# Kernel tuning notes

Measured on AMD Instinct MI355X. Metric: run time of the kernel, lower is better.

The kernel has to match this reference:

```python
import jax, jax.numpy as jnp
import numpy as np

B = 32; C = 3; IMG = 224; P = 16; G = IMG // P  # 14x14 patches
N = G * G + 1  # 197 tokens incl cls
D = 768; L = 12; H = 12; HD = D // H; FF = 4 * D
NR = (2 * G - 1) * (2 * G - 1) + 3  # 732
SCALE = HD ** -0.5


def _rel_index():
    ch = np.arange(G); cw = np.arange(G)
    coords = np.stack(np.meshgrid(ch, cw, indexing='ij')).reshape(2, -1)
    rel = (coords[:, :, None] - coords[:, None, :]).transpose(1, 2, 0).copy()
    rel[:, :, 0] += G - 1
    rel[:, :, 1] += G - 1
    rel[:, :, 0] *= 2 * G - 1
    idx = np.zeros((N, N), dtype=np.int32)
    idx[1:, 1:] = rel.sum(-1)
    idx[0, :] = NR - 3
    idx[:, 0] = NR - 2
    idx[0, 0] = NR - 1
    return jnp.asarray(idx)


def setup_inputs() -> dict:
    key = jax.random.key(0)
    ks = jax.random.split(key, 10)
    def nrm(k, shape, s=0.02):
        return jax.random.normal(k, shape, jnp.float32) * s
    return {
        'x': jax.random.normal(ks[0], (B, C, IMG, IMG), jnp.float32),
        'patch_w': nrm(ks[1], (D, C, P, P)),
        'patch_b': jnp.zeros((D,), jnp.float32),
        'cls_token': nrm(ks[2], (1, 1, D)),
        'ln1_g': jnp.ones((L, D), jnp.float32), 'ln1_b': jnp.zeros((L, D), jnp.float32),
        'qkv_w': nrm(ks[3], (L, 3 * D, D)),
        'q_bias': jnp.zeros((L, D), jnp.float32), 'v_bias': jnp.zeros((L, D), jnp.float32),
        'rel_table': nrm(ks[4], (L, NR, H)),
        'proj_w': nrm(ks[5], (L, D, D)), 'proj_b': jnp.zeros((L, D), jnp.float32),
        'gamma1': 0.1 * jnp.ones((L, D), jnp.float32),
        'ln2_g': jnp.ones((L, D), jnp.float32), 'ln2_b': jnp.zeros((L, D), jnp.float32),
        'fc1_w': nrm(ks[6], (L, FF, D)), 'fc1_b': jnp.zeros((L, FF), jnp.float32),
        'fc2_w': nrm(ks[7], (L, D, FF)), 'fc2_b': jnp.zeros((L, D), jnp.float32),
        'gamma2': 0.1 * jnp.ones((L, D), jnp.float32),
        'fcn_g': jnp.ones((D,), jnp.float32), 'fcn_b': jnp.zeros((D,), jnp.float32),
        'rel_index': _rel_index(),
    }


def _ln(x, g, b):
    m = x.mean(-1, keepdims=True)
    v = ((x - m) ** 2).mean(-1, keepdims=True)
    return (x - m) * jax.lax.rsqrt(v + 1e-5) * g + b


def reference(x, patch_w, patch_b, cls_token, ln1_g, ln1_b, qkv_w, q_bias, v_bias,
              rel_table, proj_w, proj_b, gamma1, ln2_g, ln2_b, fc1_w, fc1_b,
              fc2_w, fc2_b, gamma2, fcn_g, fcn_b, rel_index):
    b = x.shape[0]
    # patch embed: stride-P conv == unfold + matmul
    xp = x.reshape(b, C, G, P, G, P).transpose(0, 2, 4, 1, 3, 5).reshape(b, G * G, C * P * P)
    tok = xp @ patch_w.reshape(D, C * P * P).T + patch_b  # [B, 196, D]
    tok = jnp.concatenate([jnp.broadcast_to(cls_token, (b, 1, D)), tok], axis=1)  # [B, N, D]

    def block(t, p):
        g1, b1, qw, qb, vb, rt, pw, pb, gm1, g2, b2, f1w, f1b, f2w, f2b, gm2 = p
        h = _ln(t, g1, b1)
        qkv_bias = jnp.concatenate([qb, jnp.zeros_like(qb), vb])
        qkv = (h @ qw.T + qkv_bias).reshape(b, N, 3, H, HD).transpose(2, 0, 3, 1, 4)
        q, k, v = qkv[0] * SCALE, qkv[1], qkv[2]  # [B,H,N,HD]
        rpb = jnp.transpose(rt[rel_index], (2, 0, 1))  # [H,N,N]
        attn = jax.nn.softmax(jnp.einsum('bhid,bhjd->bhij', q, k) + rpb[None], axis=-1)
        o = jnp.einsum('bhij,bhjd->bhid', attn, v).transpose(0, 2, 1, 3).reshape(b, N, D)
        t = t + gm1 * (o @ pw.T + pb)
        h2 = _ln(t, g2, b2)
        m = jax.nn.gelu(h2 @ f1w.T + f1b, approximate=False) @ f2w.T + f2b
        return t + gm2 * m, None

    params = (ln1_g, ln1_b, qkv_w, q_bias, v_bias, rel_table, proj_w, proj_b,
              gamma1, ln2_g, ln2_b, fc1_w, fc1_b, fc2_w, fc2_b, gamma2)
    tok, _ = jax.lax.scan(block, tok, params)
    # BEiT-style mean pooling over patch tokens + fc_norm
    return _ln(tok[:, 1:].mean(axis=1), fcn_g, fcn_b)  # [B, D]
```

## Files before the change

kernel.cpp:

```cpp
#include <hip/hip_runtime.h>


#define BATCH 32
#define NTOK 197
#define NLAYER 12
#define NRR 732
#define MROWS (BATCH * NTOK)
#define MPAD 6400

#define NKV 224
#define QT_N 13
#define VSTR 232
#define PSTR 232
#define RPB_PER_LH (QT_N * 14 * 4 * 16 * 4)
#define RPB_PER_L (RPB_PER_LH * 12)
#define WL_ELEMS 8257536

typedef __attribute__((ext_vector_type(8))) short bf16x8_t;
typedef __attribute__((ext_vector_type(4))) float f32x4_t;

__device__ __forceinline__ unsigned short f2bf_rn(float f) {
  unsigned u = __float_as_uint(f);
  unsigned r = (u + 0x7FFFu + ((u >> 16) & 1u)) >> 16;
  return (unsigned short)r;
}
__device__ __forceinline__ float bf2f(unsigned short u) {
  return __uint_as_float(((unsigned)u) << 16);
}

__device__ __forceinline__ void gld16(const unsigned short* g, unsigned short* l) {
  __builtin_amdgcn_global_load_lds(
      (const __attribute__((address_space(1))) unsigned int*)g,
      (__attribute__((address_space(3))) unsigned int*)l, 16, 0, 0);
}

__global__ void cvt4(const float4* __restrict__ s, ushort4* __restrict__ d, int n4) {
  int i = blockIdx.x * 256 + threadIdx.x;
  if (i >= n4) return;
  float4 v = s[i];
  ushort4 r;
  r.x = f2bf_rn(v.x); r.y = f2bf_rn(v.y); r.z = f2bf_rn(v.z); r.w = f2bf_rn(v.w);
  d[i] = r;
}

__global__ void cvt_layer(const float4* __restrict__ qw, const float4* __restrict__ pw,
                          const float4* __restrict__ f1, const float4* __restrict__ f2,
                          ushort4* __restrict__ dst) {
  const int n_q = 2304 * 768 / 4;
  const int n_p = 768 * 768 / 4;
  const int n_1 = 3072 * 768 / 4;
  int i = blockIdx.x * 256 + threadIdx.x;
  float4 v;
  if (i < n_q) v = qw[i];
  else if (i < n_q + n_p) v = pw[i - n_q];
  else if (i < n_q + n_p + n_1) v = f1[i - n_q - n_p];
  else if (i < n_q + n_p + 2 * n_1) v = f2[i - n_q - n_p - n_1];
  else return;
  ushort4 r;
  r.x = f2bf_rn(v.x); r.y = f2bf_rn(v.y); r.z = f2bf_rn(v.z); r.w = f2bf_rn(v.w);
  dst[i] = r;
}

__global__ void build_rpb(const float* __restrict__ rt, const int* __restrict__ ridx,
                          unsigned short* __restrict__ dst) {
  int idx = blockIdx.x * 256 + threadIdx.x;
  if (idx >= RPB_PER_L * NLAYER) return;
  int r = idx & 3;
  int fr = (idx >> 2) & 15;
  int fq = (idx >> 6) & 3;
  int t2 = idx >> 8;
  int jt = t2 % 14; t2 /= 14;
  int qt = t2 % QT_N; t2 /= QT_N;
  int h = t2 % 12;
  int l = t2 / 12;
  int row = qt * 16 + fq * 4 + r;
  int col = jt * 16 + fr;
  float v = -30000.f;
  if (row < 197 && col < 197)
    v = rt[((size_t)l * NRR + ridx[row * 197 + col]) * 12 + h];
  dst[idx] = f2bf_rn(v);
}

__global__ void build_xp(const float* __restrict__ x, unsigned short* __restrict__ xp) {
  int idx = blockIdx.x * 256 + threadIdx.x;
  if (idx >= 6272 * 768) return;
  int r = idx / 768, c = idx - r * 768;
  int b = r / 196, p = r - b * 196;
  int gy = p / 14, gx = p - gy * 14;
  int ch = c >> 8, rem = c & 255, py = rem >> 4, px = rem & 15;
  float v = x[(((size_t)b * 3 + ch) * 224 + gy * 16 + py) * 224 + gx * 16 + px];
  xp[(size_t)(b * 197 + 1 + p) * 768 + c] = f2bf_rn(v);
}

__global__ void fill_cls(const float* __restrict__ cls, float* __restrict__ tok) {
  int idx = blockIdx.x * 256 + threadIdx.x;
  int b = idx / 768, d = idx - b * 768;
  tok[(size_t)(b * 197) * 768 + d] = cls[d];
}

__global__ __launch_bounds__(256) void ln_rows(const float* __restrict__ x,
                                               unsigned short* __restrict__ y,
                                               const float* __restrict__ g,
                                               const float* __restrict__ b) {
  int row = blockIdx.x;
  const float* xr = x + (size_t)row * 768;
  int t = threadIdx.x;
  float v0 = xr[t], v1 = xr[t + 256], v2 = xr[t + 512];
  float s = v0 + v1 + v2;
  float q = v0 * v0 + v1 * v1 + v2 * v2;
  for (int off = 32; off; off >>= 1) { s += __shfl_xor(s, off); q += __shfl_xor(q, off); }
  __shared__ float rs[4], rq[4];
  int wave = t >> 6;
  if ((t & 63) == 0) { rs[wave] = s; rq[wave] = q; }
  __syncthreads();
  s = rs[0] + rs[1] + rs[2] + rs[3];
  q = rq[0] + rq[1] + rq[2] + rq[3];
  float mean = s * (1.f / 768.f);
  float var = q * (1.f / 768.f) - mean * mean;
  float rstd = rsqrtf(var + 1e-5f);
  unsigned short* yr = y + (size_t)row * 768;
  yr[t]       = f2bf_rn((v0 - mean) * rstd * g[t]       + b[t]);
  yr[t + 256] = f2bf_rn((v1 - mean) * rstd * g[t + 256] + b[t + 256]);
  yr[t + 512] = f2bf_rn((v2 - mean) * rstd * g[t + 512] + b[t + 512]);
}

template <int MODE, int BM>
__global__ __launch_bounds__(256, 2) void gemm_t(
    const unsigned short* __restrict__ A, const unsigned short* __restrict__ Bw,
    float* __restrict__ Cf, unsigned short* __restrict__ Cb,
    const float* __restrict__ bias, const float* __restrict__ bias2,
    const float* __restrict__ gamma, int K, int N) {
  constexpr int MI = BM / 32;
  __shared__ __align__(16) unsigned short As[2][BM * 32];
  __shared__ __align__(16) unsigned short Bs[2][128 * 32];
  const int tid = threadIdx.x;
  const int wave = tid >> 6, lane = tid & 63;
  const int m0 = blockIdx.y * BM, n0 = blockIdx.x * 128;
  const int wm = (wave & 1) * (MI * 16), wn = (wave >> 1) * 64;
  f32x4_t acc[MI][4] = {};
  const int srow = lane >> 2;
  const int scol = ((lane & 3) ^ ((lane >> 3) & 3)) * 8;
  const unsigned short* Abase = A + (size_t)(m0 + srow) * K + scol;
  const unsigned short* Bbase = Bw + (size_t)(n0 + srow) * K + scol;
  const int fr = lane & 15, fq = lane >> 4;
  const int rchunk = (fq ^ ((fr >> 1) & 3)) * 8;
  for (int k0 = 0; k0 < K; k0 += 64) {
    __syncthreads();
#pragma unroll
    for (int s = 0; s < 2; ++s) {
#pragma unroll
      for (int u0 = 0; u0 < BM / 64; ++u0) {
        int u = wave + u0 * 4;
        gld16(Abase + (size_t)(u * 16) * K + k0 + s * 32, &As[s][u * 512]);
      }
#pragma unroll
      for (int u0 = 0; u0 < 2; ++u0) {
        int u = wave + u0 * 4;
        gld16(Bbase + (size_t)(u * 16) * K + k0 + s * 32, &Bs[s][u * 512]);
      }
    }
    __syncthreads();
#pragma unroll
    for (int s = 0; s < 2; ++s) {
      bf16x8_t af[MI], bfr[4];
#pragma unroll
      for (int i = 0; i < MI; ++i)
        af[i] = *(const bf16x8_t*)(&As[s][(wm + i * 16 + fr) * 32 + rchunk]);
#pragma unroll
      for (int j = 0; j < 4; ++j)
        bfr[j] = *(const bf16x8_t*)(&Bs[s][(wn + j * 16 + fr) * 32 + rchunk]);
#pragma unroll
      for (int i = 0; i < MI; ++i)
#pragma unroll
        for (int j = 0; j < 4; ++j)
          acc[i][j] = __builtin_amdgcn_mfma_f32_16x16x32_bf16(af[i], bfr[j], acc[i][j], 0, 0, 0);
    }
  }
  const int er = (lane >> 4) * 4;
  const int ec = lane & 15;
#pragma unroll
  for (int i = 0; i < MI; ++i) {
#pragma unroll
    for (int j = 0; j < 4; ++j) {
#pragma unroll
      for (int r = 0; r < 4; ++r) {
        int row = m0 + wm + i * 16 + er + r;
        int col = n0 + wn + j * 16 + ec;
        float v = acc[i][j][r];
        size_t idx = (size_t)row * N + col;
        if constexpr (MODE == 0) {
          Cf[idx] = v + bias[col];
        } else if constexpr (MODE == 1) {
          float bv = (col < 768) ? bias[col] : (col >= 1536 ? bias2[col - 1536] : 0.f);
          v += bv;
          if (col < 768) v *= 0.125f;
          Cb[idx] = f2bf_rn(v);
        } else if constexpr (MODE == 2) {
          Cf[idx] = Cf[idx] + gamma[col] * (v + bias[col]);
        } else {
          float tt = v + bias[col];
          float gv = 0.5f * tt * (1.f + erff(tt * 0.70710678118654752f));
          Cb[idx] = f2bf_rn(gv);
        }
      }
    }
  }
}

__global__ __launch_bounds__(256) void attn_mfma(
    const unsigned short* __restrict__ qkv,
    const unsigned short* __restrict__ rpb,
    unsigned short* __restrict__ o) {
  const int bh = blockIdx.x;
  const int b = bh / 12, h = bh - b * 12;
  __shared__ __align__(16) unsigned short Vt[64 * VSTR];
  __shared__ __align__(16) unsigned short Pls[4][16 * PSTR];
  const int t = threadIdx.x;
  const int wave = t >> 6, lane = t & 63;
  const int fr = lane & 15, fq = lane >> 4;
  const size_t qbase = (size_t)(b * 197) * 2304 + h * 64;
  const unsigned short* rph = rpb + (size_t)h * RPB_PER_LH;

  for (int idx = t; idx < NKV * 16; idx += 256) {
    int j = idx >> 4, d0 = (idx & 15) * 4;
    ushort4 v = *(const ushort4*)(qkv + qbase + 1536 + (size_t)j * 2304 + d0);
    Vt[(d0 + 0) * VSTR + j] = v.x;
    Vt[(d0 + 1) * VSTR + j] = v.y;
    Vt[(d0 + 2) * VSTR + j] = v.z;
    Vt[(d0 + 3) * VSTR + j] = v.w;
  }
  __syncthreads();

  unsigned short* P = &Pls[wave][0];
  for (int qt = wave; qt < QT_N; qt += 4) {
    const unsigned short* qrow = qkv + qbase + (size_t)(qt * 16 + fr) * 2304 + fq * 8;
    bf16x8_t qa0 = *(const bf16x8_t*)(qrow);
    bf16x8_t qa1 = *(const bf16x8_t*)(qrow + 32);
    f32x4_t S[14];
#pragma unroll
    for (int jt = 0; jt < 14; ++jt) {
      const unsigned short* krow = qkv + qbase + 768 + (size_t)(jt * 16 + fr) * 2304 + fq * 8;
      bf16x8_t kb0 = *(const bf16x8_t*)(krow);
      bf16x8_t kb1 = *(const bf16x8_t*)(krow + 32);
      f32x4_t s = {};
      s = __builtin_amdgcn_mfma_f32_16x16x32_bf16(qa0, kb0, s, 0, 0, 0);
      s = __builtin_amdgcn_mfma_f32_16x16x32_bf16(qa1, kb1, s, 0, 0, 0);
      ushort4 rb = *(const ushort4*)(rph + ((size_t)(qt * 14 + jt) * 4 + fq) * 64 + fr * 4);
      s[0] += bf2f(rb.x); s[1] += bf2f(rb.y); s[2] += bf2f(rb.z); s[3] += bf2f(rb.w);
      S[jt] = s;
    }
    float mx[4], sum[4];
#pragma unroll
    for (int r = 0; r < 4; ++r) mx[r] = S[0][r];
#pragma unroll
    for (int jt = 1; jt < 14; ++jt)
#pragma unroll
      for (int r = 0; r < 4; ++r) mx[r] = fmaxf(mx[r], S[jt][r]);
#pragma unroll
    for (int r = 0; r < 4; ++r) {
      for (int off = 1; off < 16; off <<= 1) mx[r] = fmaxf(mx[r], __shfl_xor(mx[r], off));
      sum[r] = 0.f;
    }
#pragma unroll
    for (int jt = 0; jt < 14; ++jt) {
#pragma unroll
      for (int r = 0; r < 4; ++r) {
        float p = __expf(S[jt][r] - mx[r]);
        sum[r] += p;
        P[(fq * 4 + r) * PSTR + jt * 16 + fr] = f2bf_rn(p);
      }
    }
    float rinv[4];
#pragma unroll
    for (int r = 0; r < 4; ++r) {
      for (int off = 1; off < 16; off <<= 1) sum[r] += __shfl_xor(sum[r], off);
      rinv[r] = 1.f / sum[r];
    }
    bf16x8_t pa[7];
#pragma unroll
    for (int ks = 0; ks < 7; ++ks)
      pa[ks] = *(const bf16x8_t*)(P + fr * PSTR + ks * 32 + fq * 8);
#pragma unroll
    for (int nt = 0; nt < 4; ++nt) {
      f32x4_t O = {};
#pragma unroll
      for (int ks = 0; ks < 7; ++ks) {
        bf16x8_t vb = *(const bf16x8_t*)(Vt + (nt * 16 + fr) * VSTR + ks * 32 + fq * 8);
        O = __builtin_amdgcn_mfma_f32_16x16x32_bf16(pa[ks], vb, O, 0, 0, 0);
      }
#pragma unroll
      for (int r = 0; r < 4; ++r) {
        int row = qt * 16 + fq * 4 + r;
        if (row < 197)
          o[(size_t)(b * 197 + row) * 768 + h * 64 + nt * 16 + fr] = f2bf_rn(O[r] * rinv[r]);
      }
    }
  }
}

__global__ __launch_bounds__(256) void pool_ln(const float* __restrict__ tok,
                                               const float* __restrict__ g,
                                               const float* __restrict__ bb,
                                               float* __restrict__ out) {
  int b = blockIdx.x;
  __shared__ float pool[768];
  int t = threadIdx.x;
  for (int c = t; c < 768; c += 256) {
    float s = 0.f;
    const float* p = tok + (size_t)(b * 197 + 1) * 768 + c;
    for (int i = 0; i < 196; ++i) s += p[(size_t)i * 768];
    pool[c] = s * (1.f / 196.f);
  }
  __syncthreads();
  float s = 0.f, q = 0.f;
  for (int c = t; c < 768; c += 256) { float v = pool[c]; s += v; q += v * v; }
  for (int off = 32; off; off >>= 1) { s += __shfl_xor(s, off); q += __shfl_xor(q, off); }
  __shared__ float rs[4], rq[4];
  if ((t & 63) == 0) { rs[t >> 6] = s; rq[t >> 6] = q; }
  __syncthreads();
  s = rs[0] + rs[1] + rs[2] + rs[3];
  q = rq[0] + rq[1] + rq[2] + rq[3];
  float mean = s * (1.f / 768.f);
  float var = q * (1.f / 768.f) - mean * mean;
  float rstd = rsqrtf(var + 1e-5f);
  for (int c = t; c < 768; c += 256)
    out[(size_t)b * 768 + c] = (pool[c] - mean) * rstd * g[c] + bb[c];
}

extern "C" void kernel_launch(void* const* d_in, const int* in_sizes, int n_in,
                              void* d_out, int out_size, void* d_ws, size_t ws_size,
                              hipStream_t stream) {
  const float* x         = (const float*)d_in[0];
  const float* patch_w   = (const float*)d_in[1];
  const float* patch_b   = (const float*)d_in[2];
  const float* cls_tok   = (const float*)d_in[3];
  const float* ln1_g     = (const float*)d_in[4];
  const float* ln1_b     = (const float*)d_in[5];
  const float* qkv_w     = (const float*)d_in[6];
  const float* q_bias    = (const float*)d_in[7];
  const float* v_bias    = (const float*)d_in[8];
  const float* rel_table = (const float*)d_in[9];
  const float* proj_w    = (const float*)d_in[10];
  const float* proj_b    = (const float*)d_in[11];
  const float* gamma1    = (const float*)d_in[12];
  const float* ln2_g     = (const float*)d_in[13];
  const float* ln2_b     = (const float*)d_in[14];
  const float* fc1_w     = (const float*)d_in[15];
  const float* fc1_b     = (const float*)d_in[16];
  const float* fc2_w     = (const float*)d_in[17];
  const float* fc2_b     = (const float*)d_in[18];
  const float* gamma2    = (const float*)d_in[19];
  const float* fcn_g     = (const float*)d_in[20];
  const float* fcn_b     = (const float*)d_in[21];
  const int* rel_index   = (const int*)d_in[22];
  float* out = (float*)d_out;

  char* ws = (char*)d_ws;
  size_t off = 0;
  auto take = [&](size_t bytes) {
    char* p = ws + off;
    off += (bytes + 255) & ~(size_t)255;
    return p;
  };
  unsigned short* wl     = (unsigned short*)take((size_t)WL_ELEMS * 2);
  unsigned short* pwb    = (unsigned short*)take((size_t)589824 * 2);
  float*          tokf   = (float*)take((size_t)MPAD * 768 * 4);
  unsigned short* hb     = (unsigned short*)take((size_t)MPAD * 768 * 2);
  unsigned short* qkvb   = (unsigned short*)take((size_t)MPAD * 2304 * 2);
  unsigned short* ffb    = (unsigned short*)take((size_t)MPAD * 3072 * 2);
  unsigned short* rpbAll = (unsigned short*)take((size_t)RPB_PER_L * NLAYER * 2);
  unsigned short* xp = ffb;
  unsigned short* ob = hb;
  unsigned short* wl_qkv = wl;
  unsigned short* wl_proj = wl + (size_t)2304 * 768;
  unsigned short* wl_fc1 = wl_proj + (size_t)768 * 768;
  unsigned short* wl_fc2 = wl_fc1 + (size_t)3072 * 768;

  build_rpb<<<(RPB_PER_L * NLAYER + 255) / 256, 256, 0, stream>>>(rel_table, rel_index, rpbAll);

  cvt4<<<576, 256, 0, stream>>>((const float4*)patch_w, (ushort4*)pwb, 147456);
  build_xp<<<18816, 256, 0, stream>>>(x, xp);
  gemm_t<0, 64><<<dim3(6, 100), 256, 0, stream>>>(xp, pwb, tokf, nullptr, patch_b,
                                                  nullptr, nullptr, 768, 768);
  fill_cls<<<96, 256, 0, stream>>>(cls_tok, tokf);

  for (int l = 0; l < NLAYER; ++l) {
    cvt_layer<<<(WL_ELEMS / 4 + 255) / 256, 256, 0, stream>>>(
        (const float4*)(qkv_w + (size_t)l * 2304 * 768),
        (const float4*)(proj_w + (size_t)l * 768 * 768),
        (const float4*)(fc1_w + (size_t)l * 3072 * 768),
        (const float4*)(fc2_w + (size_t)l * 768 * 3072), (ushort4*)wl);
    ln_rows<<<MROWS, 256, 0, stream>>>(tokf, hb, ln1_g + l * 768, ln1_b + l * 768);
    gemm_t<1, 128><<<dim3(18, 50), 256, 0, stream>>>(hb, wl_qkv, nullptr, qkvb,
                                                     q_bias + l * 768, v_bias + l * 768,
                                                     nullptr, 768, 2304);
    attn_mfma<<<384, 256, 0, stream>>>(qkvb, rpbAll + (size_t)l * RPB_PER_L, ob);
    gemm_t<2, 64><<<dim3(6, 100), 256, 0, stream>>>(ob, wl_proj, tokf, nullptr,
                                                    proj_b + l * 768, nullptr,
                                                    gamma1 + l * 768, 768, 768);
    ln_rows<<<MROWS, 256, 0, stream>>>(tokf, hb, ln2_g + l * 768, ln2_b + l * 768);
    gemm_t<3, 128><<<dim3(24, 50), 256, 0, stream>>>(hb, wl_fc1, nullptr, ffb,
                                                     fc1_b + l * 3072, nullptr, nullptr,
                                                     768, 3072);
    gemm_t<2, 64><<<dim3(6, 100), 256, 0, stream>>>(ffb, wl_fc2, tokf, nullptr,
                                                    fc2_b + l * 768, nullptr,
                                                    gamma2 + l * 768, 3072, 768);
  }
  pool_ln<<<32, 256, 0, stream>>>(tokf, fcn_g, fcn_b, out);
}
```

Measured before the change: 3.361 ms.

## Double-buffer GEMM LDS tiles and remap workgroups per XCD

The GEMM main loop now double-buffers its LDS tiles: the next K-slab is loaded while MFMAs run on the current one, and there is one barrier per iteration instead of two. The launch grid becomes 1D and is remapped so that consecutive tiles land on the same XCD, which should improve L2 reuse of the A and B tiles. Occupancy hints are raised for the BM=64 variant. LDS per block doubles, which may cap occupancy below the hinted level.

```diff
diff --git a/kernel.cpp b/kernel.cpp
--- a/kernel.cpp
+++ b/kernel.cpp
@@ -125,17 +125,23 @@
 }
 
 template <int MODE, int BM>
-__global__ __launch_bounds__(256, 2) void gemm_t(
+__global__ __launch_bounds__(256, (BM == 64 ? 3 : 2)) void gemm_t(
     const unsigned short* __restrict__ A, const unsigned short* __restrict__ Bw,
     float* __restrict__ Cf, unsigned short* __restrict__ Cb,
     const float* __restrict__ bias, const float* __restrict__ bias2,
-    const float* __restrict__ gamma, int K, int N) {
+    const float* __restrict__ gamma, int K, int N, int nbx) {
   constexpr int MI = BM / 32;
-  __shared__ __align__(16) unsigned short As[2][BM * 32];
-  __shared__ __align__(16) unsigned short Bs[2][128 * 32];
+  __shared__ __align__(16) unsigned short As[2][BM * 64];
+  __shared__ __align__(16) unsigned short Bs[2][128 * 64];
   const int tid = threadIdx.x;
   const int wave = tid >> 6, lane = tid & 63;
-  const int m0 = blockIdx.y * BM, n0 = blockIdx.x * 128;
+
+  const int nwg = gridDim.x;
+  const int q8 = nwg >> 3, r8 = nwg & 7;
+  const int xcd = blockIdx.x & 7, ii = blockIdx.x >> 3;
+  const int wg = (xcd < r8 ? xcd * (q8 + 1) : r8 * (q8 + 1) + (xcd - r8) * q8) + ii;
+  const int m0 = (wg / nbx) * BM, n0 = (wg % nbx) * 128;
+
   const int wm = (wave & 1) * (MI * 16), wn = (wave >> 1) * 64;
   f32x4_t acc[MI][4] = {};
   const int srow = lane >> 2;
@@ -144,38 +150,50 @@
   const unsigned short* Bbase = Bw + (size_t)(n0 + srow) * K + scol;
   const int fr = lane & 15, fq = lane >> 4;
   const int rchunk = (fq ^ ((fr >> 1) & 3)) * 8;
-  for (int k0 = 0; k0 < K; k0 += 64) {
-    __syncthreads();
+
+  auto stage = [&](int buf, int k0) {
 #pragma unroll
     for (int s = 0; s < 2; ++s) {
 #pragma unroll
       for (int u0 = 0; u0 < BM / 64; ++u0) {
         int u = wave + u0 * 4;
-        gld16(Abase + (size_t)(u * 16) * K + k0 + s * 32, &As[s][u * 512]);
+        gld16(Abase + (size_t)(u * 16) * K + k0 + s * 32, &As[buf][s * (BM * 32) + u * 512]);
       }
 #pragma unroll
       for (int u0 = 0; u0 < 2; ++u0) {
         int u = wave + u0 * 4;
-        gld16(Bbase + (size_t)(u * 16) * K + k0 + s * 32, &Bs[s][u * 512]);
-      }
-    }
-    __syncthreads();
+        gld16(Bbase + (size_t)(u * 16) * K + k0 + s * 32, &Bs[buf][s * 4096 + u * 512]);
+      }
+    }
+  };
+
+  stage(0, 0);
+  asm volatile("s_waitcnt vmcnt(0)" ::: "memory");
+  __builtin_amdgcn_s_barrier();
+
+  const int nk = K >> 6;
+  for (int t = 0; t < nk; ++t) {
+    const int buf = t & 1;
+    if (t + 1 < nk) stage(buf ^ 1, (t + 1) << 6);
 #pragma unroll
     for (int s = 0; s < 2; ++s) {
       bf16x8_t af[MI], bfr[4];
 #pragma unroll
       for (int i = 0; i < MI; ++i)
-        af[i] = *(const bf16x8_t*)(&As[s][(wm + i * 16 + fr) * 32 + rchunk]);
+        af[i] = *(const bf16x8_t*)(&As[buf][s * (BM * 32) + (wm + i * 16 + fr) * 32 + rchunk]);
 #pragma unroll
       for (int j = 0; j < 4; ++j)
-        bfr[j] = *(const bf16x8_t*)(&Bs[s][(wn + j * 16 + fr) * 32 + rchunk]);
+        bfr[j] = *(const bf16x8_t*)(&Bs[buf][s * 4096 + (wn + j * 16 + fr) * 32 + rchunk]);
 #pragma unroll
       for (int i = 0; i < MI; ++i)
 #pragma unroll
         for (int j = 0; j < 4; ++j)
           acc[i][j] = __builtin_amdgcn_mfma_f32_16x16x32_bf16(af[i], bfr[j], acc[i][j], 0, 0, 0);
     }
-  }
+    asm volatile("s_waitcnt vmcnt(0)" ::: "memory");
+    __builtin_amdgcn_s_barrier();
+  }
+
   const int er = (lane >> 4) * 4;
   const int ec = lane & 15;
 #pragma unroll
@@ -380,8 +398,8 @@
 
   cvt4<<<576, 256, 0, stream>>>((const float4*)patch_w, (ushort4*)pwb, 147456);
   build_xp<<<18816, 256, 0, stream>>>(x, xp);
-  gemm_t<0, 64><<<dim3(6, 100), 256, 0, stream>>>(xp, pwb, tokf, nullptr, patch_b,
-                                                  nullptr, nullptr, 768, 768);
+  gemm_t<0, 64><<<600, 256, 0, stream>>>(xp, pwb, tokf, nullptr, patch_b,
+                                         nullptr, nullptr, 768, 768, 6);
   fill_cls<<<96, 256, 0, stream>>>(cls_tok, tokf);
 
   for (int l = 0; l < NLAYER; ++l) {
@@ -391,20 +409,20 @@
         (const float4*)(fc1_w + (size_t)l * 3072 * 768),
         (const float4*)(fc2_w + (size_t)l * 768 * 3072), (ushort4*)wl);
     ln_rows<<<MROWS, 256, 0, stream>>>(tokf, hb, ln1_g + l * 768, ln1_b + l * 768);
-    gemm_t<1, 128><<<dim3(18, 50), 256, 0, stream>>>(hb, wl_qkv, nullptr, qkvb,
-                                                     q_bias + l * 768, v_bias + l * 768,
-                                                     nullptr, 768, 2304);
+    gemm_t<1, 128><<<900, 256, 0, stream>>>(hb, wl_qkv, nullptr, qkvb,
+                                            q_bias + l * 768, v_bias + l * 768,
+                                            nullptr, 768, 2304, 18);
     attn_mfma<<<384, 256, 0, stream>>>(qkvb, rpbAll + (size_t)l * RPB_PER_L, ob);
-    gemm_t<2, 64><<<dim3(6, 100), 256, 0, stream>>>(ob, wl_proj, tokf, nullptr,
-                                                    proj_b + l * 768, nullptr,
-                                                    gamma1 + l * 768, 768, 768);
+    gemm_t<2, 64><<<600, 256, 0, stream>>>(ob, wl_proj, tokf, nullptr,
+                                           proj_b + l * 768, nullptr,
+                                           gamma1 + l * 768, 768, 768, 6);
     ln_rows<<<MROWS, 256, 0, stream>>>(tokf, hb, ln2_g + l * 768, ln2_b + l * 768);
-    gemm_t<3, 128><<<dim3(24, 50), 256, 0, stream>>>(hb, wl_fc1, nullptr, ffb,
-                                                     fc1_b + l * 3072, nullptr, nullptr,
-                                                     768, 3072);
-    gemm_t<2, 64><<<dim3(6, 100), 256, 0, stream>>>(ffb, wl_fc2, tokf, nullptr,
-                                                    fc2_b + l * 768, nullptr,
-                                                    gamma2 + l * 768, 3072, 768);
+    gemm_t<3, 128><<<1200, 256, 0, stream>>>(hb, wl_fc1, nullptr, ffb,
+                                             fc1_b + l * 3072, nullptr, nullptr,
+                                             768, 3072, 24);
+    gemm_t<2, 64><<<600, 256, 0, stream>>>(ffb, wl_fc2, tokf, nullptr,
+                                           fc2_b + l * 768, nullptr,
+                                           gamma2 + l * 768, 3072, 768, 6);
   }
   pool_ln<<<32, 256, 0, stream>>>(tokf, fcn_g, fcn_b, out);
 }
```

Measured after the change: 3.433 ms. 1.02x slower.
